# Performance work log

Hardware: AMD Instinct MI355X
Metric: run time of the kernel (lower is better)

The kernel has to match this reference:

```python
import jax, jax.numpy as jnp
import numpy as np


def setup_inputs() -> dict:
    key = jax.random.key(0)
    k1, k2, k3 = jax.random.split(key, 3)
    B, T, N = 2, 16, 128
    INP, COND, OUT = 64, 64, 128
    x = jax.random.normal(k1, (B, T, N, INP), dtype=jnp.float32)
    cond = jax.random.normal(k2, (B, N, N, COND), dtype=jnp.float32)
    in_dim = 6 * INP + 2 * COND  # 512
    W = jax.random.normal(k3, (in_dim, OUT), dtype=jnp.float32) / np.sqrt(in_dim)
    b = jnp.zeros((OUT,), dtype=jnp.float32)
    return {"x": x, "cond": cond, "W": W, "b": b}


def reference(x, cond, W, b):
    # x: (B,T,N,C), cond: (B,N,N,Cc), W: (6C+2Cc, O), b: (O,)
    B, T, N, C = x.shape
    Cc = cond.shape[-1]
    # temporal boundary-zeroed copies (faithful to torch cat of zeros + slices)
    x1 = x.at[:, 0].set(0.0)        # zeros at t=0
    x2 = x.at[:, -1].set(0.0)       # zeros at t=T-1
    xc = jnp.concatenate([x1, x, x2], axis=-1)  # (B,T,N,3C)
    # decompose the big linear over the concat [x1_pair, x2_pair, cond1, cond2]
    W1 = W[: 3 * C]
    W2 = W[3 * C: 6 * C]
    Wc1 = W[6 * C: 6 * C + Cc]
    Wc2 = W[6 * C + Cc:]
    a = jnp.einsum('btnc,co->btno', xc, W1)               # n1 contribution
    bpart = jnp.einsum('btnc,co->btno', xc, W2)            # n2 contribution
    # cond1[b,t,i,j] = cond[b,i,j]; cond2[b,t,i,j] = cond[b,j,i]
    cpart = (jnp.einsum('bijc,co->bijo', cond, Wc1)
             + jnp.einsum('bjic,co->bijo', cond, Wc2))     # (B,N,N,O)
    s = (a[:, :, :, None, :] + bpart[:, :, None, :, :]
         + cpart[:, None, :, :, :] + b)                    # (B,T,N,N,O)
    act = s * jax.nn.sigmoid(s)                            # swish
    return jnp.max(act, axis=3)                            # amax over n2 -> (B,T,N,O)
```

## Files before the change

### kernel.cpp

```cpp
#include <hip/hip_runtime.h>
#include <math.h>

#define B_ 2
#define T_ 16
#define N_ 128
#define CI 64
#define CO 128

#define AQ_OFF 0
#define BT_OFF 524288
#define CQ_OFF 1048576

typedef __attribute__((ext_vector_type(8))) short short8;
typedef __attribute__((ext_vector_type(4))) float f32x4;

__device__ __forceinline__ float4 f4add(float4 a, float4 b) {
  return make_float4(a.x + b.x, a.y + b.y, a.z + b.z, a.w + b.w);
}
__device__ __forceinline__ float4 f4max(float4 a, float4 b) {
  return make_float4(fmaxf(a.x, b.x), fmaxf(a.y, b.y), fmaxf(a.z, b.z), fmaxf(a.w, b.w));
}
__device__ __forceinline__ float4 f4min(float4 a, float4 b) {
  return make_float4(fminf(a.x, b.x), fminf(a.y, b.y), fminf(a.z, b.z), fminf(a.w, b.w));
}
__device__ __forceinline__ void f4fma(float4& acc, float s, float4 v) {
  acc.x = fmaf(s, v.x, acc.x);
  acc.y = fmaf(s, v.y, acc.y);
  acc.z = fmaf(s, v.z, acc.z);
  acc.w = fmaf(s, v.w, acc.w);
}
__device__ __forceinline__ float silu1(float v) { return v / (1.0f + __expf(-v)); }
__device__ __forceinline__ float4 silu4(float4 v) {
  return make_float4(silu1(v.x), silu1(v.y), silu1(v.z), silu1(v.w));
}
__device__ __forceinline__ float4 shfl4x(float4 v, int m) {
  return make_float4(__shfl_xor(v.x, m, 64), __shfl_xor(v.y, m, 64),
                     __shfl_xor(v.z, m, 64), __shfl_xor(v.w, m, 64));
}
__device__ __forceinline__ unsigned int bf2(float a, float b) {
  unsigned int ua = __float_as_uint(a);
  unsigned int ub = __float_as_uint(b);
  ua = (ua + 0x7FFFu + ((ua >> 16) & 1u)) >> 16;
  ub = (ub + 0x7FFFu + ((ub >> 16) & 1u)) >> 16;
  return (ub << 16) | ua;
}
__device__ __forceinline__ uint4 pack8(float4 lo, float4 hi) {
  return make_uint4(bf2(lo.x, lo.y), bf2(lo.z, lo.w), bf2(hi.x, hi.y), bf2(hi.z, hi.w));
}

__global__ __launch_bounds__(256) void k_ab3(
    const float* __restrict__ x, const float* __restrict__ W,
    const float* __restrict__ bias, float* __restrict__ AQ, float* __restrict__ BT)
{
  __shared__ __align__(16) float WL[64 * 128];
  __shared__ float xT[64 * 17];

  int blk = blockIdx.x;
  int nq  = blk & 7;
  int dst = (blk >> 3) & 1;
  int t   = (blk >> 4) & 15;
  int b   = blk >> 8;
  float f0 = (t != 0)      ? 1.0f : 0.0f;
  float f2 = (t != T_ - 1) ? 1.0f : 0.0f;
  int tid = threadIdx.x;

  const float4* W4 = (const float4*)W;
  float4* WL4 = (float4*)WL;
  int wb = dst * 6144;
  #pragma unroll
  for (int k = 0; k < 8; k++) {
    int idx4 = tid + k * 256;
    float4 wa = W4[wb + idx4];
    float4 wm = W4[wb + 2048 + idx4];
    float4 wc = W4[wb + 4096 + idx4];
    WL4[idx4] = make_float4(f0 * wa.x + wm.x + f2 * wc.x,
                            f0 * wa.y + wm.y + f2 * wc.y,
                            f0 * wa.z + wm.z + f2 * wc.z,
                            f0 * wa.w + wm.w + f2 * wc.w);
  }
  {
    long xb = ((long)(b * T_ + t) * N_ + nq * 16) * CI;
    #pragma unroll
    for (int k = 0; k < 4; k++) {
      int idx = tid + k * 256;
      int c = idx & 63, n = idx >> 6;
      xT[c * 17 + n] = x[xb + n * CI + c];
    }
  }
  __syncthreads();

  int nl = tid & 15;
  int qg = tid >> 4;
  float4 acc0, acc1;
  if (dst == 0) {
    acc0 = ((const float4*)bias)[qg * 2];
    acc1 = ((const float4*)bias)[qg * 2 + 1];
  } else {
    acc0 = make_float4(0, 0, 0, 0); acc1 = acc0;
  }
  #pragma unroll 8
  for (int c = 0; c < 64; c++) {
    float xv = xT[c * 17 + nl];
    float4 w0 = WL4[c * 32 + qg * 2];
    float4 w1 = WL4[c * 32 + qg * 2 + 1];
    f4fma(acc0, xv, w0);
    f4fma(acc1, xv, w1);
  }
  int n = nq * 16 + nl;
  float4* dp4 = (float4*)(dst ? BT : AQ);
  int q0 = qg * 2, q1 = qg * 2 + 1;
  long i0 = (((long)(b * 8 + (q0 >> 2)) * 16 + t) * 128 + n) * 4 + (q0 & 3);
  long i1 = (((long)(b * 8 + (q1 >> 2)) * 16 + t) * 128 + n) * 4 + (q1 & 3);
  dp4[i0] = acc0;
  dp4[i1] = acc1;
}

__global__ __launch_bounds__(256) void k_cp4b(
    const float* __restrict__ cond, const float* __restrict__ W,
    float* __restrict__ CQ)
{
  __shared__ __align__(16) unsigned char smem[49152];
  uint4* AF  = (uint4*)smem;
  uint4* WcF = (uint4*)(smem + 16384);
  float* Cp  = (float*)smem;

  int blk = blockIdx.x;
  int jh = blk & 1;
  int i  = (blk >> 1) & 127;
  int b  = blk >> 8;
  int tid = threadIdx.x;

  #pragma unroll
  for (int f = 0; f < 8; f++) {
    int fid = tid + f * 256;
    int lane_f = fid & 63;
    int ot   = (fid >> 6) & 7;
    int kh   = (fid >> 9) & 1;
    int term = fid >> 10;
    int o  = ot * 16 + (lane_f & 15);
    int kb = kh * 32 + (lane_f >> 4) * 8;
    float v[8];
    #pragma unroll
    for (int u = 0; u < 8; u++)
      v[u] = W[(384 + term * 64 + kb + u) * 128 + o];
    WcF[fid] = pack8(make_float4(v[0], v[1], v[2], v[3]),
                     make_float4(v[4], v[5], v[6], v[7]));
  }
  #pragma unroll
  for (int k = 0; k < 4; k++) {
    int idx = tid + k * 256;
    int term = idx >> 9;
    int rem = idx & 511;
    int jl = rem >> 3, oct = rem & 7;
    long row = (term == 0) ? ((long)(b * N_ + i) * N_ + jh * 64 + jl)
                           : ((long)(b * N_ + jh * 64 + jl) * N_ + i);
    const float4* src = (const float4*)(cond + row * 64 + oct * 8);
    float4 lo = src[0], hi = src[1];
    int frag = term * 512 + ((jl >> 4) * 2 + (oct >> 2)) * 64 + (oct & 3) * 16 + (jl & 15);
    AF[frag] = pack8(lo, hi);
  }
  __syncthreads();

  int lane = tid & 63;
  int w    = tid >> 6;
  f32x4 acc[8];
  #pragma unroll
  for (int ot = 0; ot < 8; ot++) {
    acc[ot][0] = 0.f; acc[ot][1] = 0.f; acc[ot][2] = 0.f; acc[ot][3] = 0.f;
  }
  const short8* AF8 = (const short8*)AF;
  const short8* WF8 = (const short8*)WcF;
  #pragma unroll
  for (int term = 0; term < 2; term++) {
    #pragma unroll
    for (int kh = 0; kh < 2; kh++) {
      short8 a = AF8[term * 512 + (w * 2 + kh) * 64 + lane];
      #pragma unroll
      for (int ot = 0; ot < 8; ot++) {
        short8 bv = WF8[((term * 2 + kh) * 8 + ot) * 64 + lane];
        acc[ot] = __builtin_amdgcn_mfma_f32_16x16x32_bf16(a, bv, acc[ot], 0, 0, 0);
      }
    }
  }
  __syncthreads();

  {
    int col = lane & 15;
    int row0 = w * 16 + (lane >> 4) * 4;
    #pragma unroll
    for (int ot = 0; ot < 8; ot++) {
      f32x4 d = acc[ot];
      int cbase = ot * 16 + col;
      Cp[(row0 + 0) * 132 + cbase] = d[0];
      Cp[(row0 + 1) * 132 + cbase] = d[1];
      Cp[(row0 + 2) * 132 + cbase] = d[2];
      Cp[(row0 + 3) * 132 + cbase] = d[3];
    }
  }
  __syncthreads();

  {
    const float4* Cp4 = (const float4*)Cp;
    float4* CQ4 = (float4*)CQ;
    int oql = tid & 3;
    int jl  = (tid >> 2) & 63;
    #pragma unroll
    for (int of_l = 0; of_l < 8; of_l++) {
      CQ4[(((long)(b * 8 + of_l) * 128) + jh * 64 + jl) * 512 + i * 4 + oql] =
          Cp4[jl * 33 + of_l * 4 + oql];
    }
  }
}

__global__ __launch_bounds__(256, 2) void k_red8(
    const float* __restrict__ AQ, const float* __restrict__ BT,
    const float* __restrict__ CQ, float* __restrict__ out)
{
  __shared__ __align__(16) float4 BtL[4096];

  int blk = blockIdx.x;
  int ih = blk & 15;
  int th = (blk >> 4) & 1;
  int of = (blk >> 5) & 7;
  int b  = blk >> 8;
  int tid = threadIdx.x;

  const float4* BT4 = (const float4*)BT;
  const float4* CQ4 = (const float4*)CQ;
  const float4* AQ4 = (const float4*)AQ;

  long btbase = ((long)(b * 8 + of) * 16 + th * 8) * 512;
  #pragma unroll
  for (int k = 0; k < 16; k++) BtL[tid + k * 256] = BT4[btbase + tid + k * 256];

  int w    = tid >> 6;
  int lane = tid & 63;
  int jh = lane >> 5;
  int il = (lane >> 2) & 7;
  int oq = lane & 3;
  int jb = w * 32 + jh * 16;

  const float4* cq = CQ4 + ((long)(b * 8 + of) * 128) * 512 + (long)(ih * 8 + il) * 4 + oq;

  float4 c[8], d[8];
  #pragma unroll
  for (int k = 0; k < 8; k++) c[k] = cq[(long)(jb + k) * 512];
  #pragma unroll
  for (int k = 0; k < 8; k++) d[k] = cq[(long)(jb + 8 + k) * 512];

  __syncthreads();

  float4 mx[8], mn[8];
  #pragma unroll
  for (int t = 0; t < 8; t++) {
    mx[t] = make_float4(-3.4e38f, -3.4e38f, -3.4e38f, -3.4e38f);
    mn[t] = make_float4(3.4e38f, 3.4e38f, 3.4e38f, 3.4e38f);
  }

  #pragma unroll
  for (int k = 0; k < 8; k++) {
    #pragma unroll
    for (int tl = 0; tl < 8; tl++) {
      float4 s = f4add(c[k], BtL[(tl * 128 + jb + k) * 4 + oq]);
      mx[tl] = f4max(mx[tl], s);
      mn[tl] = f4min(mn[tl], s);
    }
  }
  #pragma unroll
  for (int k = 0; k < 8; k++) {
    #pragma unroll
    for (int tl = 0; tl < 8; tl++) {
      float4 s = f4add(d[k], BtL[(tl * 128 + jb + 8 + k) * 4 + oq]);
      mx[tl] = f4max(mx[tl], s);
      mn[tl] = f4min(mn[tl], s);
    }
  }

  #pragma unroll
  for (int tl = 0; tl < 8; tl++) {
    mx[tl] = f4max(mx[tl], shfl4x(mx[tl], 32));
    mn[tl] = f4min(mn[tl], shfl4x(mn[tl], 32));
  }

  __syncthreads();
  float4* scr = BtL;
  if (jh == 0) {
    #pragma unroll
    for (int tl = 0; tl < 8; tl++) {
      int sidx = ((w * 8 + tl) * 8 + il) * 4 + oq;
      scr[sidx]        = mx[tl];
      scr[1024 + sidx] = mn[tl];
    }
  }
  __syncthreads();

  {
    int tl  = tid >> 5;
    int il2 = (tid >> 2) & 7;
    int oq2 = tid & 3;
    int s0 = (tl * 8 + il2) * 4 + oq2;
    float4 MX = scr[s0];
    float4 MN = scr[1024 + s0];
    #pragma unroll
    for (int ww = 1; ww < 4; ww++) {
      int si = ((ww * 8 + tl) * 8 + il2) * 4 + oq2;
      MX = f4max(MX, scr[si]);
      MN = f4min(MN, scr[1024 + si]);
    }
    int t = th * 8 + tl;
    float4 av = AQ4[(((long)(b * 8 + of) * 16 + t) * 128 + ih * 8 + il2) * 4 + oq2];
    float4 res = f4max(silu4(f4add(MX, av)), silu4(f4add(MN, av)));
    ((float4*)out)[((long)((b * 16 + t) * 128) + ih * 8 + il2) * 32 + of * 4 + oq2] = res;
  }
}

extern "C" void kernel_launch(void* const* d_in, const int* in_sizes, int n_in,
                              void* d_out, int out_size, void* d_ws, size_t ws_size,
                              hipStream_t stream) {
  const float* x    = (const float*)d_in[0];
  const float* cond = (const float*)d_in[1];
  const float* W    = (const float*)d_in[2];
  const float* bias = (const float*)d_in[3];
  float* out = (float*)d_out;

  float* ws = (float*)d_ws;
  float* AQ = ws + AQ_OFF;
  float* BT = ws + BT_OFF;
  float* CQ = ws + CQ_OFF;

  k_ab3<<<512, 256, 0, stream>>>(x, W, bias, AQ, BT);
  k_cp4b<<<512, 256, 0, stream>>>(cond, W, CQ);
  k_red8<<<512, 256, 0, stream>>>(AQ, BT, CQ, out);
}
```

Before: 93.96 us.

## Merge prep kernels into one launch, store CQ as bf16, widen reduce blocks

Folds the AB projection kernel and the cond projection kernel into a single 1024-block launch, with blocks dispatched by index, so one kernel boundary goes away. The intermediate CQ tensor is now written as packed bf16 instead of fp32, which halves the traffic of the large CQ array between the prep kernel and the reduction. The reduction kernel moves to 512 threads per block, each thread handling 8 j values instead of 16, with an eight-way cross-wave combine. The bf16 rounding of CQ adds precision loss on top of the bf16 MFMA inputs already in use.

```diff
diff --git a/kernel.cpp b/kernel.cpp
--- a/kernel.cpp
+++ b/kernel.cpp
@@ -7,9 +7,9 @@
 #define CI 64
 #define CO 128
 
-#define AQ_OFF 0
-#define BT_OFF 524288
-#define CQ_OFF 1048576
+#define AQ_OFF  0
+#define BT_OFF  524288
+#define CQB_OFF 1048576
 
 typedef __attribute__((ext_vector_type(8))) short short8;
 typedef __attribute__((ext_vector_type(4))) float f32x4;
@@ -47,174 +47,177 @@
 __device__ __forceinline__ uint4 pack8(float4 lo, float4 hi) {
   return make_uint4(bf2(lo.x, lo.y), bf2(lo.z, lo.w), bf2(hi.x, hi.y), bf2(hi.z, hi.w));
 }
-
-__global__ __launch_bounds__(256) void k_ab3(
-    const float* __restrict__ x, const float* __restrict__ W,
-    const float* __restrict__ bias, float* __restrict__ AQ, float* __restrict__ BT)
+__device__ __forceinline__ float4 unpack4(uint2 p) {
+  return make_float4(__uint_as_float(p.x << 16), __uint_as_float(p.x & 0xffff0000u),
+                     __uint_as_float(p.y << 16), __uint_as_float(p.y & 0xffff0000u));
+}
+
+__global__ __launch_bounds__(256) void k_prep3(
+    const float* __restrict__ x, const float* __restrict__ cond,
+    const float* __restrict__ W, const float* __restrict__ bias,
+    float* __restrict__ AQ, float* __restrict__ BT, unsigned int* __restrict__ CQb)
 {
-  __shared__ __align__(16) float WL[64 * 128];
-  __shared__ float xT[64 * 17];
-
+  __shared__ __align__(16) unsigned char smem[49152];
   int blk = blockIdx.x;
-  int nq  = blk & 7;
-  int dst = (blk >> 3) & 1;
-  int t   = (blk >> 4) & 15;
-  int b   = blk >> 8;
-  float f0 = (t != 0)      ? 1.0f : 0.0f;
-  float f2 = (t != T_ - 1) ? 1.0f : 0.0f;
   int tid = threadIdx.x;
 
-  const float4* W4 = (const float4*)W;
-  float4* WL4 = (float4*)WL;
-  int wb = dst * 6144;
-  #pragma unroll
-  for (int k = 0; k < 8; k++) {
-    int idx4 = tid + k * 256;
-    float4 wa = W4[wb + idx4];
-    float4 wm = W4[wb + 2048 + idx4];
-    float4 wc = W4[wb + 4096 + idx4];
-    WL4[idx4] = make_float4(f0 * wa.x + wm.x + f2 * wc.x,
-                            f0 * wa.y + wm.y + f2 * wc.y,
-                            f0 * wa.z + wm.z + f2 * wc.z,
-                            f0 * wa.w + wm.w + f2 * wc.w);
-  }
-  {
-    long xb = ((long)(b * T_ + t) * N_ + nq * 16) * CI;
+  if (blk < 512) {
+    float* WL = (float*)smem;
+    float* xT = (float*)(smem + 32768);
+
+    int nq  = blk & 7;
+    int dst = (blk >> 3) & 1;
+    int t   = (blk >> 4) & 15;
+    int b   = blk >> 8;
+    float f0 = (t != 0)      ? 1.0f : 0.0f;
+    float f2 = (t != T_ - 1) ? 1.0f : 0.0f;
+
+    const float4* W4 = (const float4*)W;
+    float4* WL4 = (float4*)WL;
+    int wb = dst * 6144;
+    #pragma unroll
+    for (int k = 0; k < 8; k++) {
+      int idx4 = tid + k * 256;
+      float4 wa = W4[wb + idx4];
+      float4 wm = W4[wb + 2048 + idx4];
+      float4 wc = W4[wb + 4096 + idx4];
+      WL4[idx4] = make_float4(f0 * wa.x + wm.x + f2 * wc.x,
+                              f0 * wa.y + wm.y + f2 * wc.y,
+                              f0 * wa.z + wm.z + f2 * wc.z,
+                              f0 * wa.w + wm.w + f2 * wc.w);
+    }
+    {
+      long xb = ((long)(b * T_ + t) * N_ + nq * 16) * CI;
+      #pragma unroll
+      for (int k = 0; k < 4; k++) {
+        int idx = tid + k * 256;
+        int c = idx & 63, n = idx >> 6;
+        xT[c * 17 + n] = x[xb + n * CI + c];
+      }
+    }
+    __syncthreads();
+
+    int nl = tid & 15;
+    int qg = tid >> 4;
+    float4 acc0, acc1;
+    if (dst == 0) {
+      acc0 = ((const float4*)bias)[qg * 2];
+      acc1 = ((const float4*)bias)[qg * 2 + 1];
+    } else {
+      acc0 = make_float4(0, 0, 0, 0); acc1 = acc0;
+    }
+    #pragma unroll 8
+    for (int c = 0; c < 64; c++) {
+      float xv = xT[c * 17 + nl];
+      float4 w0 = WL4[c * 32 + qg * 2];
+      float4 w1 = WL4[c * 32 + qg * 2 + 1];
+      f4fma(acc0, xv, w0);
+      f4fma(acc1, xv, w1);
+    }
+    int n = nq * 16 + nl;
+    float4* dp4 = (float4*)(dst ? BT : AQ);
+    int q0 = qg * 2, q1 = qg * 2 + 1;
+    long i0 = (((long)(b * 8 + (q0 >> 2)) * 16 + t) * 128 + n) * 4 + (q0 & 3);
+    long i1 = (((long)(b * 8 + (q1 >> 2)) * 16 + t) * 128 + n) * 4 + (q1 & 3);
+    dp4[i0] = acc0;
+    dp4[i1] = acc1;
+  } else {
+    uint4* AF  = (uint4*)smem;
+    uint4* WcF = (uint4*)(smem + 16384);
+    float* Cp  = (float*)smem;
+
+    int blk2 = blk - 512;
+    int jh = blk2 & 1;
+    int i  = (blk2 >> 1) & 127;
+    int b  = blk2 >> 8;
+
+    #pragma unroll
+    for (int f = 0; f < 8; f++) {
+      int fid = tid + f * 256;
+      int lane_f = fid & 63;
+      int ot   = (fid >> 6) & 7;
+      int kh   = (fid >> 9) & 1;
+      int term = fid >> 10;
+      int o  = ot * 16 + (lane_f & 15);
+      int kb = kh * 32 + (lane_f >> 4) * 8;
+      float v[8];
+      #pragma unroll
+      for (int u = 0; u < 8; u++)
+        v[u] = W[(384 + term * 64 + kb + u) * 128 + o];
+      WcF[fid] = pack8(make_float4(v[0], v[1], v[2], v[3]),
+                       make_float4(v[4], v[5], v[6], v[7]));
+    }
     #pragma unroll
     for (int k = 0; k < 4; k++) {
       int idx = tid + k * 256;
-      int c = idx & 63, n = idx >> 6;
-      xT[c * 17 + n] = x[xb + n * CI + c];
-    }
-  }
-  __syncthreads();
-
-  int nl = tid & 15;
-  int qg = tid >> 4;
-  float4 acc0, acc1;
-  if (dst == 0) {
-    acc0 = ((const float4*)bias)[qg * 2];
-    acc1 = ((const float4*)bias)[qg * 2 + 1];
-  } else {
-    acc0 = make_float4(0, 0, 0, 0); acc1 = acc0;
-  }
-  #pragma unroll 8
-  for (int c = 0; c < 64; c++) {
-    float xv = xT[c * 17 + nl];
-    float4 w0 = WL4[c * 32 + qg * 2];
-    float4 w1 = WL4[c * 32 + qg * 2 + 1];
-    f4fma(acc0, xv, w0);
-    f4fma(acc1, xv, w1);
-  }
-  int n = nq * 16 + nl;
-  float4* dp4 = (float4*)(dst ? BT : AQ);
-  int q0 = qg * 2, q1 = qg * 2 + 1;
-  long i0 = (((long)(b * 8 + (q0 >> 2)) * 16 + t) * 128 + n) * 4 + (q0 & 3);
-  long i1 = (((long)(b * 8 + (q1 >> 2)) * 16 + t) * 128 + n) * 4 + (q1 & 3);
-  dp4[i0] = acc0;
-  dp4[i1] = acc1;
-}
-
-__global__ __launch_bounds__(256) void k_cp4b(
-    const float* __restrict__ cond, const float* __restrict__ W,
-    float* __restrict__ CQ)
-{
-  __shared__ __align__(16) unsigned char smem[49152];
-  uint4* AF  = (uint4*)smem;
-  uint4* WcF = (uint4*)(smem + 16384);
-  float* Cp  = (float*)smem;
-
-  int blk = blockIdx.x;
-  int jh = blk & 1;
-  int i  = (blk >> 1) & 127;
-  int b  = blk >> 8;
-  int tid = threadIdx.x;
-
-  #pragma unroll
-  for (int f = 0; f < 8; f++) {
-    int fid = tid + f * 256;
-    int lane_f = fid & 63;
-    int ot   = (fid >> 6) & 7;
-    int kh   = (fid >> 9) & 1;
-    int term = fid >> 10;
-    int o  = ot * 16 + (lane_f & 15);
-    int kb = kh * 32 + (lane_f >> 4) * 8;
-    float v[8];
-    #pragma unroll
-    for (int u = 0; u < 8; u++)
-      v[u] = W[(384 + term * 64 + kb + u) * 128 + o];
-    WcF[fid] = pack8(make_float4(v[0], v[1], v[2], v[3]),
-                     make_float4(v[4], v[5], v[6], v[7]));
-  }
-  #pragma unroll
-  for (int k = 0; k < 4; k++) {
-    int idx = tid + k * 256;
-    int term = idx >> 9;
-    int rem = idx & 511;
-    int jl = rem >> 3, oct = rem & 7;
-    long row = (term == 0) ? ((long)(b * N_ + i) * N_ + jh * 64 + jl)
-                           : ((long)(b * N_ + jh * 64 + jl) * N_ + i);
-    const float4* src = (const float4*)(cond + row * 64 + oct * 8);
-    float4 lo = src[0], hi = src[1];
-    int frag = term * 512 + ((jl >> 4) * 2 + (oct >> 2)) * 64 + (oct & 3) * 16 + (jl & 15);
-    AF[frag] = pack8(lo, hi);
-  }
-  __syncthreads();
-
-  int lane = tid & 63;
-  int w    = tid >> 6;
-  f32x4 acc[8];
-  #pragma unroll
-  for (int ot = 0; ot < 8; ot++) {
-    acc[ot][0] = 0.f; acc[ot][1] = 0.f; acc[ot][2] = 0.f; acc[ot][3] = 0.f;
-  }
-  const short8* AF8 = (const short8*)AF;
-  const short8* WF8 = (const short8*)WcF;
-  #pragma unroll
-  for (int term = 0; term < 2; term++) {
-    #pragma unroll
-    for (int kh = 0; kh < 2; kh++) {
-      short8 a = AF8[term * 512 + (w * 2 + kh) * 64 + lane];
+      int term = idx >> 9;
+      int rem = idx & 511;
+      int jl = rem >> 3, oct = rem & 7;
+      long row = (term == 0) ? ((long)(b * N_ + i) * N_ + jh * 64 + jl)
+                             : ((long)(b * N_ + jh * 64 + jl) * N_ + i);
+      const float4* src = (const float4*)(cond + row * 64 + oct * 8);
+      float4 lo = src[0], hi = src[1];
+      int frag = term * 512 + ((jl >> 4) * 2 + (oct >> 2)) * 64 + (oct & 3) * 16 + (jl & 15);
+      AF[frag] = pack8(lo, hi);
+    }
+    __syncthreads();
+
+    int lane = tid & 63;
+    int w    = tid >> 6;
+    f32x4 acc[8];
+    #pragma unroll
+    for (int ot = 0; ot < 8; ot++) {
+      acc[ot][0] = 0.f; acc[ot][1] = 0.f; acc[ot][2] = 0.f; acc[ot][3] = 0.f;
+    }
+    const short8* AF8 = (const short8*)AF;
+    const short8* WF8 = (const short8*)WcF;
+    #pragma unroll
+    for (int term = 0; term < 2; term++) {
+      #pragma unroll
+      for (int kh = 0; kh < 2; kh++) {
+        short8 a = AF8[term * 512 + (w * 2 + kh) * 64 + lane];
+        #pragma unroll
+        for (int ot = 0; ot < 8; ot++) {
+          short8 bv = WF8[((term * 2 + kh) * 8 + ot) * 64 + lane];
+          acc[ot] = __builtin_amdgcn_mfma_f32_16x16x32_bf16(a, bv, acc[ot], 0, 0, 0);
+        }
+      }
+    }
+    __syncthreads();
+
+    {
+      int col = lane & 15;
+      int row0 = w * 16 + (lane >> 4) * 4;
       #pragma unroll
       for (int ot = 0; ot < 8; ot++) {
-        short8 bv = WF8[((term * 2 + kh) * 8 + ot) * 64 + lane];
-        acc[ot] = __builtin_amdgcn_mfma_f32_16x16x32_bf16(a, bv, acc[ot], 0, 0, 0);
+        f32x4 d = acc[ot];
+        int cbase = ot * 16 + col;
+        Cp[(row0 + 0) * 132 + cbase] = d[0];
+        Cp[(row0 + 1) * 132 + cbase] = d[1];
+        Cp[(row0 + 2) * 132 + cbase] = d[2];
+        Cp[(row0 + 3) * 132 + cbase] = d[3];
       }
     }
-  }
-  __syncthreads();
-
-  {
-    int col = lane & 15;
-    int row0 = w * 16 + (lane >> 4) * 4;
-    #pragma unroll
-    for (int ot = 0; ot < 8; ot++) {
-      f32x4 d = acc[ot];
-      int cbase = ot * 16 + col;
-      Cp[(row0 + 0) * 132 + cbase] = d[0];
-      Cp[(row0 + 1) * 132 + cbase] = d[1];
-      Cp[(row0 + 2) * 132 + cbase] = d[2];
-      Cp[(row0 + 3) * 132 + cbase] = d[3];
-    }
-  }
-  __syncthreads();
-
-  {
-    const float4* Cp4 = (const float4*)Cp;
-    float4* CQ4 = (float4*)CQ;
-    int oql = tid & 3;
-    int jl  = (tid >> 2) & 63;
-    #pragma unroll
-    for (int of_l = 0; of_l < 8; of_l++) {
-      CQ4[(((long)(b * 8 + of_l) * 128) + jh * 64 + jl) * 512 + i * 4 + oql] =
-          Cp4[jl * 33 + of_l * 4 + oql];
-    }
-  }
-}
-
-__global__ __launch_bounds__(256, 2) void k_red8(
+    __syncthreads();
+
+    {
+      const float4* Cp4 = (const float4*)Cp;
+      uint2* CQ2 = (uint2*)CQb;
+      int oql = tid & 3;
+      int jl  = (tid >> 2) & 63;
+      #pragma unroll
+      for (int of_l = 0; of_l < 8; of_l++) {
+        float4 v = Cp4[jl * 33 + of_l * 4 + oql];
+        CQ2[(((long)(b * 8 + of_l) * 128) + jh * 64 + jl) * 512 + i * 4 + oql] =
+            make_uint2(bf2(v.x, v.y), bf2(v.z, v.w));
+      }
+    }
+  }
+}
+
+__global__ __launch_bounds__(512, 4) void k_red9(
     const float* __restrict__ AQ, const float* __restrict__ BT,
-    const float* __restrict__ CQ, float* __restrict__ out)
+    const unsigned int* __restrict__ CQb, float* __restrict__ out)
 {
   __shared__ __align__(16) float4 BtL[4096];
 
@@ -226,28 +229,24 @@
   int tid = threadIdx.x;
 
   const float4* BT4 = (const float4*)BT;
-  const float4* CQ4 = (const float4*)CQ;
+  const uint2*  CQ2 = (const uint2*)CQb;
   const float4* AQ4 = (const float4*)AQ;
-
-  long btbase = ((long)(b * 8 + of) * 16 + th * 8) * 512;
-  #pragma unroll
-  for (int k = 0; k < 16; k++) BtL[tid + k * 256] = BT4[btbase + tid + k * 256];
 
   int w    = tid >> 6;
   int lane = tid & 63;
   int jh = lane >> 5;
   int il = (lane >> 2) & 7;
   int oq = lane & 3;
-  int jb = w * 32 + jh * 16;
-
-  const float4* cq = CQ4 + ((long)(b * 8 + of) * 128) * 512 + (long)(ih * 8 + il) * 4 + oq;
-
-  float4 c[8], d[8];
-  #pragma unroll
-  for (int k = 0; k < 8; k++) c[k] = cq[(long)(jb + k) * 512];
-  #pragma unroll
-  for (int k = 0; k < 8; k++) d[k] = cq[(long)(jb + 8 + k) * 512];
-
+  int jb = w * 16 + jh * 8;
+
+  const uint2* cq = CQ2 + ((long)(b * 8 + of) * 128) * 512 + (long)(ih * 8 + il) * 4 + oq;
+  uint2 cb[8];
+  #pragma unroll
+  for (int k = 0; k < 8; k++) cb[k] = cq[(long)(jb + k) * 512];
+
+  long btbase = ((long)(b * 8 + of) * 16 + th * 8) * 512;
+  #pragma unroll
+  for (int k = 0; k < 8; k++) BtL[tid + k * 512] = BT4[btbase + tid + k * 512];
   __syncthreads();
 
   float4 mx[8], mn[8];
@@ -259,18 +258,10 @@
 
   #pragma unroll
   for (int k = 0; k < 8; k++) {
+    float4 c = unpack4(cb[k]);
     #pragma unroll
     for (int tl = 0; tl < 8; tl++) {
-      float4 s = f4add(c[k], BtL[(tl * 128 + jb + k) * 4 + oq]);
-      mx[tl] = f4max(mx[tl], s);
-      mn[tl] = f4min(mn[tl], s);
-    }
-  }
-  #pragma unroll
-  for (int k = 0; k < 8; k++) {
-    #pragma unroll
-    for (int tl = 0; tl < 8; tl++) {
-      float4 s = f4add(d[k], BtL[(tl * 128 + jb + 8 + k) * 4 + oq]);
+      float4 s = f4add(c, BtL[(tl * 128 + jb + k) * 4 + oq]);
       mx[tl] = f4max(mx[tl], s);
       mn[tl] = f4min(mn[tl], s);
     }
@@ -289,23 +280,23 @@
     for (int tl = 0; tl < 8; tl++) {
       int sidx = ((w * 8 + tl) * 8 + il) * 4 + oq;
       scr[sidx]        = mx[tl];
-      scr[1024 + sidx] = mn[tl];
+      scr[2048 + sidx] = mn[tl];
     }
   }
   __syncthreads();
 
-  {
+  if (tid < 256) {
     int tl  = tid >> 5;
     int il2 = (tid >> 2) & 7;
     int oq2 = tid & 3;
     int s0 = (tl * 8 + il2) * 4 + oq2;
     float4 MX = scr[s0];
-    float4 MN = scr[1024 + s0];
-    #pragma unroll
-    for (int ww = 1; ww < 4; ww++) {
+    float4 MN = scr[2048 + s0];
+    #pragma unroll
+    for (int ww = 1; ww < 8; ww++) {
       int si = ((ww * 8 + tl) * 8 + il2) * 4 + oq2;
       MX = f4max(MX, scr[si]);
-      MN = f4min(MN, scr[1024 + si]);
+      MN = f4min(MN, scr[2048 + si]);
     }
     int t = th * 8 + tl;
     float4 av = AQ4[(((long)(b * 8 + of) * 16 + t) * 128 + ih * 8 + il2) * 4 + oq2];
@@ -326,9 +317,8 @@
   float* ws = (float*)d_ws;
   float* AQ = ws + AQ_OFF;
   float* BT = ws + BT_OFF;
-  float* CQ = ws + CQ_OFF;
-
-  k_ab3<<<512, 256, 0, stream>>>(x, W, bias, AQ, BT);
-  k_cp4b<<<512, 256, 0, stream>>>(cond, W, CQ);
-  k_red8<<<512, 256, 0, stream>>>(AQ, BT, CQ, out);
-}
+  unsigned int* CQb = (unsigned int*)(ws + CQB_OFF);
+
+  k_prep3<<<1024, 256, 0, stream>>>(x, cond, W, bias, AQ, BT, CQb);
+  k_red9<<<512, 512, 0, stream>>>(AQ, BT, CQb, out);
+}
```

After: 95.33 us. No clear change (+1.5%).
